# Optimization experiments

Measured on AMD Instinct MI355X. Metric: run time of the kernel, lower is better.

Reference implementation:

```python
import jax, jax.numpy as jnp
import numpy as np

GROUPS = 16
EPS = 1e-6


def conv1x1(x, w, b):
    # x: (B,C,N,K), w: (O,C), b: (O,)
    return jnp.einsum('oc,bcnk->bonk', w, x) + b[None, :, None, None]


def group_norm(x, gamma, beta):
    # GroupNorm(16, C, eps=1e-6, affine=True) over (C/g, N, K) per sample
    B, C, N, K = x.shape
    xg = x.reshape(B, GROUPS, C // GROUPS, N, K)
    mu = xg.mean(axis=(2, 3, 4), keepdims=True)
    var = xg.var(axis=(2, 3, 4), keepdims=True)
    xn = ((xg - mu) * jax.lax.rsqrt(var + EPS)).reshape(B, C, N, K)
    return xn * gamma[None, :, None, None] + beta[None, :, None, None]


def _gather_nbrs(x, idx):
    # x: (B,C,N), idx: (B,N,K) -> (B,C,N,K)
    return jax.vmap(lambda xb, ib: xb[:, ib])(x, idx)


def lse(coords_t, feats, idx, dist, w, b, g, bt):
    # LocalSpatialEncoding: coords_t (B,3,N), feats (B,C,N,1)
    nbr_coords = _gather_nbrs(coords_t, idx)                       # (B,3,N,K)
    ctr_coords = jnp.broadcast_to(coords_t[..., None], nbr_coords.shape)
    concat = jnp.concatenate(
        [ctr_coords, nbr_coords, ctr_coords - nbr_coords, dist[:, None]], axis=1)  # (B,10,N,K)
    enc = jax.nn.relu(group_norm(conv1x1(concat, w, b), g, bt))    # (B,C,N,K)
    nbr_feats = _gather_nbrs(feats[..., 0], idx)                   # (B,C,N,K)
    return jnp.concatenate([enc, nbr_feats], axis=1)               # (B,2C,N,K)


def attentive_pool(x, w, b, g, bt):
    # mean over K, then SharedMLP with GN+ReLU -> (B,O,N,1)
    m = x.mean(axis=-1, keepdims=True)
    return jax.nn.relu(group_norm(conv1x1(m, w, b), g, bt))


def setup_inputs() -> dict:
    B, N, K, D_IN, D_OUT = 2, 32768, 16, 72, 64
    H = D_OUT // 2  # 32
    key = jax.random.key(0)
    ks = jax.random.split(key, 24)

    def w(k, o, i):
        return jax.random.normal(k, (o, i), jnp.float32) * (1.0 / np.sqrt(i))

    inp = {
        'coords': jax.random.normal(ks[0], (B, N, 3), jnp.float32),
        'features': jax.random.normal(ks[1], (B, D_IN, N, 1), jnp.float32),
        'idx': jax.random.randint(ks[2], (B, N, K), 0, N, jnp.int32),
        'dist': jax.random.uniform(ks[3], (B, N, K), jnp.float32),
        # mlp1: d_in -> d_out//2, LeakyReLU(0.2)
        'w_mlp1': w(ks[4], H, D_IN), 'b_mlp1': jnp.zeros((H,), jnp.float32),
        # lse1 mlp: 10 -> H, GN+ReLU
        'w_lse1': w(ks[5], H, 10), 'b_lse1': jnp.zeros((H,), jnp.float32),
        'g_lse1': jnp.ones((H,), jnp.float32), 'bt_lse1': jnp.zeros((H,), jnp.float32),
        # pool1: d_out -> H, GN+ReLU
        'w_pool1': w(ks[6], H, D_OUT), 'b_pool1': jnp.zeros((H,), jnp.float32),
        'g_pool1': jnp.ones((H,), jnp.float32), 'bt_pool1': jnp.zeros((H,), jnp.float32),
        # lse2 mlp: 10 -> H
        'w_lse2': w(ks[7], H, 10), 'b_lse2': jnp.zeros((H,), jnp.float32),
        'g_lse2': jnp.ones((H,), jnp.float32), 'bt_lse2': jnp.zeros((H,), jnp.float32),
        # pool2: d_out -> d_out
        'w_pool2': w(ks[8], D_OUT, D_OUT), 'b_pool2': jnp.zeros((D_OUT,), jnp.float32),
        'g_pool2': jnp.ones((D_OUT,), jnp.float32), 'bt_pool2': jnp.zeros((D_OUT,), jnp.float32),
        # mlp2: d_out -> 2*d_out (no bn, no act)
        'w_mlp2': w(ks[9], 2 * D_OUT, D_OUT), 'b_mlp2': jnp.zeros((2 * D_OUT,), jnp.float32),
        # shortcut: d_in -> 2*d_out, GN, no act
        'w_sc': w(ks[10], 2 * D_OUT, D_IN), 'b_sc': jnp.zeros((2 * D_OUT,), jnp.float32),
        'g_sc': jnp.ones((2 * D_OUT,), jnp.float32), 'bt_sc': jnp.zeros((2 * D_OUT,), jnp.float32),
    }
    return inp


def reference(coords, features, idx, dist,
              w_mlp1, b_mlp1,
              w_lse1, b_lse1, g_lse1, bt_lse1,
              w_pool1, b_pool1, g_pool1, bt_pool1,
              w_lse2, b_lse2, g_lse2, bt_lse2,
              w_pool2, b_pool2, g_pool2, bt_pool2,
              w_mlp2, b_mlp2,
              w_sc, b_sc, g_sc, bt_sc):
    coords_t = coords.transpose(0, 2, 1)                        # (B,3,N)
    x = jax.nn.leaky_relu(conv1x1(features, w_mlp1, b_mlp1), 0.2)   # (B,32,N,1)
    x = lse(coords_t, x, idx, dist, w_lse1, b_lse1, g_lse1, bt_lse1)  # (B,64,N,K)
    x = attentive_pool(x, w_pool1, b_pool1, g_pool1, bt_pool1)        # (B,32,N,1)
    x = lse(coords_t, x, idx, dist, w_lse2, b_lse2, g_lse2, bt_lse2)  # (B,64,N,K)
    x = attentive_pool(x, w_pool2, b_pool2, g_pool2, bt_pool2)        # (B,64,N,1)
    main = conv1x1(x, w_mlp2, b_mlp2)                                 # (B,128,N,1)
    sc = group_norm(conv1x1(features, w_sc, b_sc), g_sc, bt_sc)       # (B,128,N,1)
    return jax.nn.leaky_relu(main + sc, 0.01)
```

## Files before the change

kernel.cpp:

```cpp
#include <hip/hip_runtime.h>
#include <hip/hip_fp16.h>

#define NN 32768
#define GEPS 1e-6f

__device__ __forceinline__ float wredsum(float v){
  v += __shfl_xor(v, 32); v += __shfl_xor(v, 16); v += __shfl_xor(v, 8);
  v += __shfl_xor(v, 4);  v += __shfl_xor(v, 2);  v += __shfl_xor(v, 1);
  return v;
}
__device__ __forceinline__ float eredsum(float v){
  v += __shfl_xor(v, 8); v += __shfl_xor(v, 16); v += __shfl_xor(v, 32);
  return v;
}
__device__ __forceinline__ float ecomb(float v){
  v += __shfl_xor(v, 1); v += __shfl_xor(v, 2); v += __shfl_xor(v, 4);
  return v;
}

__global__ void __launch_bounds__(256) f0_prep(
    const float* __restrict__ w_mlp1, const float* __restrict__ b_mlp1,
    const float* __restrict__ w_sc,   const float* __restrict__ b_sc,
    const float* __restrict__ w_pool1,const float* __restrict__ w_pool2,
    float* __restrict__ WallT, float* __restrict__ ball,
    float* __restrict__ wp1T,  float* __restrict__ wp2T)
{
  const int t0 = blockIdx.x*256 + threadIdx.x;
  const int stride = gridDim.x*256;
  for (int u=t0; u<72*160; u+=stride){
    int i = u/160, o = u - i*160;
    WallT[u] = (o < 128) ? w_sc[o*72+i] : w_mlp1[(o-128)*72+i];
  }
  for (int u=t0; u<160; u+=stride)
    ball[u] = (u < 128) ? b_sc[u] : b_mlp1[u-128];
  for (int u=t0; u<64*32; u+=stride){ int c=u>>5, o=u&31; wp1T[u] = w_pool1[o*64+c]; }
  for (int u=t0; u<64*64; u+=stride){ int c=u>>6, o=u&63; wp2T[u] = w_pool2[o*64+c]; }
}

__global__ void __launch_bounds__(256,2) k0_mlp1_scstats(
    const float* __restrict__ feat, const float* __restrict__ WallT,
    const float* __restrict__ ball,
    __half* __restrict__ X1, float* __restrict__ scS, float* __restrict__ scQ)
{
  __shared__ float xl[72][128];
  __shared__ float wl[72*32];
  __shared__ float ssl[128], sql[128];
  const int tid = threadIdx.x, lane = tid & 63;
  const int wid = __builtin_amdgcn_readfirstlane(tid >> 6);
  const int b   = __builtin_amdgcn_readfirstlane((int)blockIdx.x >> 8);
  const int n0  = ((int)blockIdx.x & 255) << 7;
  const int p0  = lane*2;

  for (int u=tid; u<72*128; u+=256){
    int c = u>>7, j = u&127;
    xl[c][j] = feat[(size_t)(b*72+c)*NN + n0 + j];
  }

#pragma unroll 1
  for (int pass=0; pass<5; ++pass){
    __syncthreads();
    for (int u=tid; u<2304; u+=256){
      int i = u>>5, c = u&31;
      wl[u] = WallT[i*160 + pass*32 + c];
    }
    __syncthreads();

    const int oc = pass*32 + wid*8;
    float a0[8], a1[8];
#pragma unroll
    for (int q=0;q<8;q++){ float bv = ball[oc+q]; a0[q]=bv; a1[q]=bv; }

    const float* wbase = wl + wid*8;
#pragma unroll
    for (int i=0;i<72;i++){
      const float2 x2 = *(const float2*)&xl[i][p0];
      const float4 w0 = *(const float4*)(wbase + i*32);
      const float4 w1 = *(const float4*)(wbase + i*32 + 4);
      a0[0]=fmaf(w0.x,x2.x,a0[0]); a1[0]=fmaf(w0.x,x2.y,a1[0]);
      a0[1]=fmaf(w0.y,x2.x,a0[1]); a1[1]=fmaf(w0.y,x2.y,a1[1]);
      a0[2]=fmaf(w0.z,x2.x,a0[2]); a1[2]=fmaf(w0.z,x2.y,a1[2]);
      a0[3]=fmaf(w0.w,x2.x,a0[3]); a1[3]=fmaf(w0.w,x2.y,a1[3]);
      a0[4]=fmaf(w1.x,x2.x,a0[4]); a1[4]=fmaf(w1.x,x2.y,a1[4]);
      a0[5]=fmaf(w1.y,x2.x,a0[5]); a1[5]=fmaf(w1.y,x2.y,a1[5]);
      a0[6]=fmaf(w1.z,x2.x,a0[6]); a1[6]=fmaf(w1.z,x2.y,a1[6]);
      a0[7]=fmaf(w1.w,x2.x,a0[7]); a1[7]=fmaf(w1.w,x2.y,a1[7]);
    }

    if (pass < 4){
#pragma unroll
      for (int q=0;q<8;q++){
        float s  = wredsum(a0[q]+a1[q]);
        float s2 = wredsum(a0[q]*a0[q] + a1[q]*a1[q]);
        if (lane==0){ ssl[oc+q] = s; sql[oc+q] = s2; }
      }
    } else {
      __syncthreads();
      float* xst = &xl[0][0];
#pragma unroll
      for (int q=0;q<8;q++){
        float v0 = a0[q], v1 = a1[q];
        v0 = v0 > 0.f ? v0 : 0.2f*v0;
        v1 = v1 > 0.f ? v1 : 0.2f*v1;
        float2 t; t.x=v0; t.y=v1;
        *(float2*)&xst[(wid*8+q)*130 + p0] = t;
      }
      __syncthreads();
      __half* xb = X1 + ((size_t)b*NN + n0)*32;
#pragma unroll
      for (int r=0;r<2;r++){
        int u = tid + r*256;
        int p = u>>2, co = (u&3)*8;
        __half2 h[4];
        h[0] = __floats2half2_rn(xst[(co+0)*130+p], xst[(co+1)*130+p]);
        h[1] = __floats2half2_rn(xst[(co+2)*130+p], xst[(co+3)*130+p]);
        h[2] = __floats2half2_rn(xst[(co+4)*130+p], xst[(co+5)*130+p]);
        h[3] = __floats2half2_rn(xst[(co+6)*130+p], xst[(co+7)*130+p]);
        *(uint4*)(xb + (size_t)p*32 + co) = *(uint4*)h;
      }
    }
  }

  if (tid < 128){
    atomicAdd(&scS[b*128+tid], ssl[tid]);
    atomicAdd(&scQ[b*128+tid], sql[tid]);
  }
}

__global__ void __launch_bounds__(256) k1_vmom(
    const float* __restrict__ coords, const int* __restrict__ idx,
    const float* __restrict__ dist, float* __restrict__ vm)
{
  __shared__ float red[4*65];
  const int tid = threadIdx.x, lane = tid & 63, wid = tid >> 6;
  const int gn = blockIdx.x*256 + tid;
  const int pt = gn >> 2, h = gn & 3;
  const int b = pt >> 15, n = pt & (NN-1);
  const size_t pb = (size_t)b*NN + n;
  const float c0 = coords[pb*3+0], c1 = coords[pb*3+1], c2 = coords[pb*3+2];

  int ja[4]; float da[4];
  {
    int4 j4 = *(const int4*)(idx + pb*16 + h*4);
    float4 d4 = *(const float4*)(dist + pb*16 + h*4);
    ja[0]=j4.x; ja[1]=j4.y; ja[2]=j4.z; ja[3]=j4.w;
    da[0]=d4.x; da[1]=d4.y; da[2]=d4.z; da[3]=d4.w;
  }

  float aS[10], aM[55];
#pragma unroll
  for (int i=0;i<10;i++) aS[i]=0.f;
#pragma unroll
  for (int i=0;i<55;i++) aM[i]=0.f;

#pragma unroll
  for (int k=0;k<4;k++){
    const float* nb = coords + ((size_t)b*NN + ja[k])*3;
    const float n0v=nb[0], n1v=nb[1], n2v=nb[2];
    const float v[10] = {c0,c1,c2,n0v,n1v,n2v,c0-n0v,c1-n1v,c2-n2v,da[k]};
#pragma unroll
    for (int i=0;i<10;i++){
      aS[i] += v[i];
#pragma unroll
      for (int j=i;j<10;j++)
        aM[i*10 - (i*(i-1))/2 + (j-i)] += v[i]*v[j];
    }
  }

#pragma unroll
  for (int i=0;i<10;i++){ float s = wredsum(aS[i]); if (lane==0) red[wid*65+i] = s; }
#pragma unroll
  for (int i=0;i<55;i++){ float s = wredsum(aM[i]); if (lane==0) red[wid*65+10+i] = s; }
  __syncthreads();
  if (tid < 65){
    float s = red[tid] + red[65+tid] + red[130+tid] + red[195+tid];
    const int bb = blockIdx.x >> 9;
    atomicAdd(&vm[bb*65+tid], s);
  }
}

__global__ void f1_fold(
    const float* __restrict__ w_lse1, const float* __restrict__ b_lse1,
    const float* __restrict__ g_lse1, const float* __restrict__ bt_lse1,
    const float* __restrict__ w_lse2, const float* __restrict__ b_lse2,
    const float* __restrict__ g_lse2, const float* __restrict__ bt_lse2,
    const float* __restrict__ vm,
    float* __restrict__ w1p, float* __restrict__ w2p)
{
  const int tid = threadIdx.x;
  const int half = tid >> 6;
  const int u = tid & 63, b = u >> 5, c = u & 31;
  const float* W  = half ? w_lse2  : w_lse1;
  const float* Bv = half ? b_lse2  : b_lse1;
  const float* G  = half ? g_lse2  : g_lse1;
  const float* Bt = half ? bt_lse2 : bt_lse1;
  float wr[10];
#pragma unroll
  for (int i=0;i<10;i++) wr[i] = W[c*10+i];
  const float* S = vm + b*65;
  const float* M = vm + b*65 + 10;
  float P = 0.f;
#pragma unroll
  for (int i=0;i<10;i++) P = fmaf(wr[i], S[i], P);
  float Q = 0.f;
#pragma unroll
  for (int i=0;i<10;i++){
#pragma unroll
    for (int j=i;j<10;j++){
      float m = M[i*10 - (i*(i-1))/2 + (j-i)];
      float t = wr[i]*wr[j]*m;
      Q += (i==j) ? t : 2.f*t;
    }
  }
  const float invNK = 1.f/((float)NN*16.f);
  const float bc = Bv[c];
  float mean = P*invNK + bc;
  float ey2  = (Q + 2.f*bc*P)*invNK + bc*bc;
  float mu = 0.5f*(mean + __shfl_xor(mean,1));
  float e2 = 0.5f*(ey2  + __shfl_xor(ey2, 1));
  float var = e2 - mu*mu;
  float rstd = rsqrtf(var + GEPS);
  float a = G[c]*rstd, d = Bt[c] - mu*a;
  float* out = (half ? w2p : w1p) + (b*32+c)*12;
#pragma unroll
  for (int i=0;i<10;i++) out[i] = wr[i]*a;
  out[10] = bc*a + d;
  out[11] = 0.f;
}

__global__ void __launch_bounds__(256,6) k2_lse1_pool1(
    const float* __restrict__ coords, const int* __restrict__ idx,
    const float* __restrict__ dist, const __half* __restrict__ X1,
    const float* __restrict__ w1p, const float* __restrict__ wp1T,
    const float* __restrict__ b_pool1,
    __half* __restrict__ Y1, float* __restrict__ p1S, float* __restrict__ p1Q)
{
  __shared__ float mfl[32*66];
  __shared__ float wlds[64*32];
  __shared__ float sl[32], ql[32];
  const int tid = threadIdx.x, lane = tid & 63;
  const int e = tid & 7;
  const int pl = tid >> 3;
  if (tid < 32){ sl[tid]=0.f; ql[tid]=0.f; }
  for (int u=tid; u<2048; u+=256) wlds[u] = wp1T[u];
  __syncthreads();
  const int b = __builtin_amdgcn_readfirstlane((int)blockIdx.x & 1);
  const int n = (((int)blockIdx.x >> 1) << 5) + pl;
  const size_t pb = (size_t)b*NN + n;
  float* mf = &mfl[pl*66];
  const float s16 = 0.0625f;

  {
    int ja[16];
    const int4* ip = (const int4*)(idx + pb*16);
#pragma unroll
    for (int k4=0;k4<4;k4++){
      int4 j4 = ip[k4];
      ja[k4*4+0]=j4.x; ja[k4*4+1]=j4.y; ja[k4*4+2]=j4.z; ja[k4*4+3]=j4.w;
    }
    float af0=0.f, af1=0.f, af2=0.f, af3=0.f;
    const __half* xb = X1 + (size_t)b*NN*32 + e*4;
#pragma unroll 4
    for (int k=0;k<16;k++){
      uint2 v = *(const uint2*)(xb + (size_t)ja[k]*32);
      __half2 h0 = *(__half2*)&v.x, h1 = *(__half2*)&v.y;
      float2 f0 = __half22float2(h0), f1 = __half22float2(h1);
      af0+=f0.x; af1+=f0.y; af2+=f1.x; af3+=f1.y;
    }
    mf[32+e*4+0]=af0*s16; mf[32+e*4+1]=af1*s16;
    mf[32+e*4+2]=af2*s16; mf[32+e*4+3]=af3*s16;
  }

  {
    int2 j2 = *(const int2*)(idx + pb*16 + e*2);
    float2 d2 = *(const float2*)(dist + pb*16 + e*2);
    const float* nb0 = coords + ((size_t)b*NN + j2.x)*3;
    const float* nb1 = coords + ((size_t)b*NN + j2.y)*3;
    const float nx0=nb0[0], ny0=nb0[1], nz0=nb0[2];
    const float nx1=nb1[0], ny1=nb1[1], nz1=nb1[2];
    const float c0=coords[pb*3], c1=coords[pb*3+1], c2=coords[pb*3+2];
    const float* wrow = w1p + (size_t)(b*32)*12;
#pragma unroll 1
    for (int cc=0;cc<4;cc++){
      float ptc[8];
#pragma unroll
      for (int q=0;q<8;q++){
        const float4* r4 = (const float4*)(wrow + (cc*8+q)*12);
        float4 ra=r4[0], rb=r4[1], rc=r4[2];
        const float t0=ra.x+rb.z, t1=ra.y+rb.w, t2=ra.z+rc.x;
        const float u0=ra.w-rb.z, u1=rb.x-rb.w, u2=rb.y-rc.x;
        const float wd=rc.y;
        float cb = rc.z;
        cb = fmaf(t0,c0,cb); cb = fmaf(t1,c1,cb); cb = fmaf(t2,c2,cb);
        float s0 = cb, s1 = cb;
        s0 = fmaf(u0,nx0,s0); s0 = fmaf(u1,ny0,s0); s0 = fmaf(u2,nz0,s0);
        s0 = fmaf(wd,d2.x,s0);
        s1 = fmaf(u0,nx1,s1); s1 = fmaf(u1,ny1,s1); s1 = fmaf(u2,nz1,s1);
        s1 = fmaf(wd,d2.y,s1);
        ptc[q] = fmaxf(s0,0.f) + fmaxf(s1,0.f);
      }
#pragma unroll
      for (int q=0;q<8;q++) ptc[q] = ecomb(ptc[q]);
      if ((e>>1)==cc){
        float v0 = (e&1) ? ptc[4] : ptc[0];
        float v1 = (e&1) ? ptc[5] : ptc[1];
        float v2 = (e&1) ? ptc[6] : ptc[2];
        float v3 = (e&1) ? ptc[7] : ptc[3];
        mf[e*4+0]=v0*s16; mf[e*4+1]=v1*s16;
        mf[e*4+2]=v2*s16; mf[e*4+3]=v3*s16;
      }
    }
  }
  __syncthreads();

  const int o0 = e*4;
  float yac[4];
  {
    const float4 b0 = *(const float4*)(b_pool1 + o0);
    yac[0]=b0.x; yac[1]=b0.y; yac[2]=b0.z; yac[3]=b0.w;
  }
#pragma unroll 4
  for (int c=0;c<64;c++){
    const float mc = mf[c];
    const float4 w0 = *(const float4*)(wlds + c*32 + o0);
    yac[0]=fmaf(w0.x,mc,yac[0]); yac[1]=fmaf(w0.y,mc,yac[1]);
    yac[2]=fmaf(w0.z,mc,yac[2]); yac[3]=fmaf(w0.w,mc,yac[3]);
  }
  {
    __half2 h[2];
    h[0] = __floats2half2_rn(yac[0], yac[1]);
    h[1] = __floats2half2_rn(yac[2], yac[3]);
    *(uint2*)(Y1 + pb*32 + o0) = *(uint2*)h;
  }
#pragma unroll
  for (int q=0;q<4;q++){
    float s  = eredsum(yac[q]);
    float s2 = eredsum(yac[q]*yac[q]);
    if (lane < 8){ atomicAdd(&sl[o0+q], s); atomicAdd(&ql[o0+q], s2); }
  }
  __syncthreads();
  if (tid<32){ atomicAdd(&p1S[b*32+tid], sl[tid]); atomicAdd(&p1Q[b*32+tid], ql[tid]); }
}

__global__ void __launch_bounds__(256,6) k4_lse2_pool2(
    const float* __restrict__ coords, const int* __restrict__ idx,
    const float* __restrict__ dist, const __half* __restrict__ Y1,
    const float* __restrict__ w2p, const float* __restrict__ wp2T,
    const float* __restrict__ b_pool2,
    const float* __restrict__ p1S, const float* __restrict__ p1Q,
    const float* __restrict__ g_p1, const float* __restrict__ bt_p1,
    float* __restrict__ Y2T, float* __restrict__ p2S, float* __restrict__ p2Q)
{
  __shared__ float mfl[32*66];
  __shared__ float wlds[64*64];
  __shared__ float sl[64], ql[64];
  __shared__ float al[32], dl[32];
  const int tid = threadIdx.x, lane = tid & 63;
  const int e = tid & 7;
  const int pl = tid >> 3;
  const int b = __builtin_amdgcn_readfirstlane((int)blockIdx.x & 1);
  if (tid < 64){ sl[tid]=0.f; ql[tid]=0.f; }
  if (tid >= 64 && tid < 96){
    const int c = tid - 64;
    float s = p1S[b*32+c], q = p1Q[b*32+c];
    s += __shfl_xor(s,1); q += __shfl_xor(q,1);
    const float inv = 1.f/(2.f*(float)NN);
    float mu = s*inv, e2 = q*inv, var = e2-mu*mu;
    float rstd = rsqrtf(var + GEPS);
    float a = g_p1[c]*rstd;
    al[c] = a; dl[c] = bt_p1[c] - mu*a;
  }
  for (int u=tid; u<4096; u+=256) wlds[u] = wp2T[u];
  __syncthreads();
  const int n0g = (((int)blockIdx.x >> 1) << 5);
  const int n = n0g + pl;
  const size_t pb = (size_t)b*NN + n;
  float* mf = &mfl[pl*66];
  const float s16 = 0.0625f;

  {
    const float a0g=al[e*4+0], a1g=al[e*4+1], a2g=al[e*4+2], a3g=al[e*4+3];
    const float d0g=dl[e*4+0], d1g=dl[e*4+1], d2g=dl[e*4+2], d3g=dl[e*4+3];
    int ja[16];
    const int4* ip = (const int4*)(idx + pb*16);
#pragma unroll
    for (int k4=0;k4<4;k4++){
      int4 j4 = ip[k4];
      ja[k4*4+0]=j4.x; ja[k4*4+1]=j4.y; ja[k4*4+2]=j4.z; ja[k4*4+3]=j4.w;
    }
    float af0=0.f, af1=0.f, af2=0.f, af3=0.f;
    const __half* yb = Y1 + (size_t)b*NN*32 + e*4;
#pragma unroll 4
    for (int k=0;k<16;k++){
      uint2 v = *(const uint2*)(yb + (size_t)ja[k]*32);
      __half2 h0 = *(__half2*)&v.x, h1 = *(__half2*)&v.y;
      float2 f0 = __half22float2(h0), f1 = __half22float2(h1);
      af0 += fmaxf(fmaf(f0.x, a0g, d0g), 0.f);
      af1 += fmaxf(fmaf(f0.y, a1g, d1g), 0.f);
      af2 += fmaxf(fmaf(f1.x, a2g, d2g), 0.f);
      af3 += fmaxf(fmaf(f1.y, a3g, d3g), 0.f);
    }
    mf[32+e*4+0]=af0*s16; mf[32+e*4+1]=af1*s16;
    mf[32+e*4+2]=af2*s16; mf[32+e*4+3]=af3*s16;
  }

  {
    int2 j2 = *(const int2*)(idx + pb*16 + e*2);
    float2 d2 = *(const float2*)(dist + pb*16 + e*2);
    const float* nb0 = coords + ((size_t)b*NN + j2.x)*3;
    const float* nb1 = coords + ((size_t)b*NN + j2.y)*3;
    const float nx0=nb0[0], ny0=nb0[1], nz0=nb0[2];
    const float nx1=nb1[0], ny1=nb1[1], nz1=nb1[2];
    const float c0=coords[pb*3], c1=coords[pb*3+1], c2=coords[pb*3+2];
    const float* wrow = w2p + (size_t)(b*32)*12;
#pragma unroll 1
    for (int cc=0;cc<4;cc++){
      float ptc[8];
#pragma unroll
      for (int q=0;q<8;q++){
        const float4* r4 = (const float4*)(wrow + (cc*8+q)*12);
        float4 ra=r4[0], rb=r4[1], rc=r4[2];
        const float t0=ra.x+rb.z, t1=ra.y+rb.w, t2=ra.z+rc.x;
        const float u0=ra.w-rb.z, u1=rb.x-rb.w, u2=rb.y-rc.x;
        const float wd=rc.y;
        float cb = rc.z;
        cb = fmaf(t0,c0,cb); cb = fmaf(t1,c1,cb); cb = fmaf(t2,c2,cb);
        float s0 = cb, s1 = cb;
        s0 = fmaf(u0,nx0,s0); s0 = fmaf(u1,ny0,s0); s0 = fmaf(u2,nz0,s0);
        s0 = fmaf(wd,d2.x,s0);
        s1 = fmaf(u0,nx1,s1); s1 = fmaf(u1,ny1,s1); s1 = fmaf(u2,nz1,s1);
        s1 = fmaf(wd,d2.y,s1);
        ptc[q] = fmaxf(s0,0.f) + fmaxf(s1,0.f);
      }
#pragma unroll
      for (int q=0;q<8;q++) ptc[q] = ecomb(ptc[q]);
      if ((e>>1)==cc){
        float v0 = (e&1) ? ptc[4] : ptc[0];
        float v1 = (e&1) ? ptc[5] : ptc[1];
        float v2 = (e&1) ? ptc[6] : ptc[2];
        float v3 = (e&1) ? ptc[7] : ptc[3];
        mf[e*4+0]=v0*s16; mf[e*4+1]=v1*s16;
        mf[e*4+2]=v2*s16; mf[e*4+3]=v3*s16;
      }
    }
  }
  __syncthreads();

  const int o0 = e*8;
  float yac[8];
  {
    const float4 b0 = *(const float4*)(b_pool2 + o0);
    const float4 b1 = *(const float4*)(b_pool2 + o0 + 4);
    yac[0]=b0.x; yac[1]=b0.y; yac[2]=b0.z; yac[3]=b0.w;
    yac[4]=b1.x; yac[5]=b1.y; yac[6]=b1.z; yac[7]=b1.w;
  }
#pragma unroll 4
  for (int c=0;c<64;c++){
    const float mc = mf[c];
    const float4 w0 = *(const float4*)(wlds + c*64 + o0);
    const float4 w1 = *(const float4*)(wlds + c*64 + o0 + 4);
    yac[0]=fmaf(w0.x,mc,yac[0]); yac[1]=fmaf(w0.y,mc,yac[1]);
    yac[2]=fmaf(w0.z,mc,yac[2]); yac[3]=fmaf(w0.w,mc,yac[3]);
    yac[4]=fmaf(w1.x,mc,yac[4]); yac[5]=fmaf(w1.y,mc,yac[5]);
    yac[6]=fmaf(w1.z,mc,yac[6]); yac[7]=fmaf(w1.w,mc,yac[7]);
  }
#pragma unroll
  for (int q=0;q<8;q++){
    float s  = eredsum(yac[q]);
    float s2 = eredsum(yac[q]*yac[q]);
    if (lane < 8){ atomicAdd(&sl[o0+q], s); atomicAdd(&ql[o0+q], s2); }
  }
  __syncthreads();
  float* ldsT = &mfl[0];
#pragma unroll
  for (int o=0;o<8;o++) ldsT[(o0+o)*33 + pl] = yac[o];
  __syncthreads();
#pragma unroll
  for (int r=0;r<8;r++){
    int u = tid + r*256;
    int ch = u >> 5, p = u & 31;
    Y2T[((size_t)(b*64+ch))*NN + n0g + p] = ldsT[ch*33 + p];
  }
  if (tid<64){ atomicAdd(&p2S[b*64+tid], sl[tid]); atomicAdd(&p2Q[b*64+tid], ql[tid]); }
}

__global__ void f3a_affines(
    const float* __restrict__ scS, const float* __restrict__ scQ,
    const float* __restrict__ g_sc, const float* __restrict__ bt_sc,
    const float* __restrict__ b_sc, const float* __restrict__ b_mlp2,
    const float* __restrict__ p2S, const float* __restrict__ p2Q,
    const float* __restrict__ g_p2, const float* __restrict__ bt_p2,
    float* __restrict__ ascT, float* __restrict__ cstF,
    float* __restrict__ a2F, float* __restrict__ d2F)
{
  const int tid = threadIdx.x;
  if (tid < 256){
    const int b = tid >> 7, c = tid & 127;
    float s = scS[b*128+c], q = scQ[b*128+c];
    s += __shfl_xor(s,1); q += __shfl_xor(q,1);
    s += __shfl_xor(s,2); q += __shfl_xor(q,2);
    s += __shfl_xor(s,4); q += __shfl_xor(q,4);
    const float inv = 1.f/(8.f*(float)NN);
    float mu = s*inv, e2 = q*inv, var = e2-mu*mu;
    float rstd = rsqrtf(var + GEPS);
    float a = g_sc[c]*rstd;
    ascT[tid] = a;
    cstF[tid] = b_mlp2[c] + a*b_sc[c] + (bt_sc[c] - mu*a);
  } else {
    const int t = tid - 256;
    const int b = t >> 6, c = t & 63;
    float s = p2S[b*64+c], q = p2Q[b*64+c];
    s += __shfl_xor(s,1); q += __shfl_xor(q,1);
    s += __shfl_xor(s,2); q += __shfl_xor(q,2);
    const float inv = 1.f/(4.f*(float)NN);
    float mu = s*inv, e2 = q*inv, var = e2-mu*mu;
    float rstd = rsqrtf(var + GEPS);
    float a = g_p2[c]*rstd;
    a2F[t] = a; d2F[t] = bt_p2[c] - mu*a;
  }
}

__global__ void __launch_bounds__(256) f3b_wcomb(
    const float* __restrict__ w_mlp2, const float* __restrict__ w_sc,
    const float* __restrict__ ascT, float* __restrict__ Wcomb)
{
  const int t0 = blockIdx.x*256 + threadIdx.x;
  const int stride = gridDim.x*256;
  for (int u=t0; u<2*136*128; u+=stride){
    int bb = u / 17408;
    int rr = u - bb*17408;
    int i = rr >> 7, o = rr & 127;
    Wcomb[u] = (i < 64) ? w_mlp2[o*64+i]
                        : w_sc[o*72 + (i-64)] * ascT[bb*128+o];
  }
}

__global__ void __launch_bounds__(256,4) k6_final(
    const float* __restrict__ feat, const float* __restrict__ Y2T,
    const float* __restrict__ Wcomb, const float* __restrict__ cstF,
    const float* __restrict__ a2F, const float* __restrict__ d2F,
    float* __restrict__ out)
{
  __shared__ float xl[34*64];
  __shared__ float wl[34*160];
  const int tid = threadIdx.x;
  const int tc = tid & 15;
  const int tp = tid >> 4;
  const int b  = __builtin_amdgcn_readfirstlane((int)blockIdx.x >> 9);
  const int n0 = ((int)blockIdx.x & 511) << 6;

  float acc[4][8];
#pragma unroll
  for (int q=0;q<8;q++){
    float bv = cstF[b*128 + tc*8 + q];
#pragma unroll
    for (int p=0;p<4;p++) acc[p][q] = bv;
  }

  const float* Wb = Wcomb + b*17408;
#pragma unroll 1
  for (int kk=0; kk<4; ++kk){
    __syncthreads();
    for (int u=tid; u<34*64; u+=256){
      int row = u>>6, j = u&63;
      int r = kk*34 + row;
      float v;
      if (r < 64){
        float y = Y2T[(size_t)(b*64+r)*NN + n0 + j];
        v = fmaxf(fmaf(y, a2F[b*64+r], d2F[b*64+r]), 0.f);
      } else {
        v = feat[(size_t)(b*72 + (r-64))*NN + n0 + j];
      }
      xl[u] = v;
    }
    for (int u=tid; u<34*128; u+=256){
      int row = u>>7, c = u&127;
      wl[row*160 + (c>>3)*10 + (c&7)] = Wb[(size_t)(kk*34+row)*128 + c];
    }
    __syncthreads();

#pragma unroll 2
    for (int i=0;i<34;i++){
      const float4 xa = *(const float4*)&xl[i*64 + tp*4];
      const float4 wa = *(const float4*)&wl[i*160 + tc*10];
      const float4 wb = *(const float4*)&wl[i*160 + tc*10 + 4];
      const float xs[4] = {xa.x,xa.y,xa.z,xa.w};
      const float wv[8] = {wa.x,wa.y,wa.z,wa.w,wb.x,wb.y,wb.z,wb.w};
#pragma unroll
      for (int p=0;p<4;p++)
#pragma unroll
        for (int q=0;q<8;q++)
          acc[p][q] = fmaf(wv[q], xs[p], acc[p][q]);
    }
  }

#pragma unroll
  for (int q=0;q<8;q++){
    const int ch = b*128 + tc*8 + q;
    float4 r0;
    float v;
    v = acc[0][q]; r0.x = v>0.f? v : 0.01f*v;
    v = acc[1][q]; r0.y = v>0.f? v : 0.01f*v;
    v = acc[2][q]; r0.z = v>0.f? v : 0.01f*v;
    v = acc[3][q]; r0.w = v>0.f? v : 0.01f*v;
    *(float4*)(out + (size_t)ch*NN + n0 + tp*4) = r0;
  }
}

extern "C" void kernel_launch(void* const* d_in, const int* in_sizes, int n_in,
                              void* d_out, int out_size, void* d_ws, size_t ws_size,
                              hipStream_t stream) {
  (void)in_sizes; (void)n_in; (void)out_size; (void)ws_size;
  const float* coords  = (const float*)d_in[0];
  const float* feats   = (const float*)d_in[1];
  const int*   idx     = (const int*)  d_in[2];
  const float* dist    = (const float*)d_in[3];
  const float* w_mlp1  = (const float*)d_in[4];
  const float* b_mlp1  = (const float*)d_in[5];
  const float* w_lse1  = (const float*)d_in[6];
  const float* b_lse1  = (const float*)d_in[7];
  const float* g_lse1  = (const float*)d_in[8];
  const float* bt_lse1 = (const float*)d_in[9];
  const float* w_pool1 = (const float*)d_in[10];
  const float* b_pool1 = (const float*)d_in[11];
  const float* g_pool1 = (const float*)d_in[12];
  const float* bt_pool1= (const float*)d_in[13];
  const float* w_lse2  = (const float*)d_in[14];
  const float* b_lse2  = (const float*)d_in[15];
  const float* g_lse2  = (const float*)d_in[16];
  const float* bt_lse2 = (const float*)d_in[17];
  const float* w_pool2 = (const float*)d_in[18];
  const float* b_pool2 = (const float*)d_in[19];
  const float* g_pool2 = (const float*)d_in[20];
  const float* bt_pool2= (const float*)d_in[21];
  const float* w_mlp2  = (const float*)d_in[22];
  const float* b_mlp2  = (const float*)d_in[23];
  const float* w_sc    = (const float*)d_in[24];
  const float* b_sc    = (const float*)d_in[25];
  const float* g_sc    = (const float*)d_in[26];
  const float* bt_sc   = (const float*)d_in[27];

  float* ws   = (float*)d_ws;
  float* scS  = ws;
  float* scQ  = ws + 256;
  float* vm   = ws + 512;
  float* p1S  = ws + 704;
  float* p1Q  = ws + 768;
  float* p2S  = ws + 832;
  float* p2Q  = ws + 960;
  float* w1p  = ws + 1280;
  float* w2p  = ws + 2048;
  float* wp1T = ws + 2816;
  float* wp2T = ws + 4864;
  float* ball = ws + 8960;
  float* cstF = ws + 9120;
  float* a2F  = ws + 9376;
  float* d2F  = ws + 9504;
  float* ascT = ws + 9632;
  float* WallT= ws + 9984;
  float* Wcomb= ws + 21504;
  __half* X1  = (__half*)(ws + 57344);
  __half* Y1  = (__half*)(ws + 57344 + (size_t)NN*32);
  float* Y2T  = ws + 57344 + (size_t)2*NN*32;

  hipMemsetAsync(d_ws, 0, 1088*sizeof(float), stream);

  f0_prep<<<32,256,0,stream>>>(w_mlp1,b_mlp1,w_sc,b_sc,w_pool1,w_pool2,
                               WallT,ball,wp1T,wp2T);
  k0_mlp1_scstats<<<512,256,0,stream>>>(feats, WallT, ball, X1, scS, scQ);
  k1_vmom<<<1024,256,0,stream>>>(coords, idx, dist, vm);
  f1_fold<<<1,128,0,stream>>>(w_lse1,b_lse1,g_lse1,bt_lse1,
                              w_lse2,b_lse2,g_lse2,bt_lse2,
                              vm, w1p, w2p);
  k2_lse1_pool1<<<2048,256,0,stream>>>(coords, idx, dist, X1, w1p, wp1T, b_pool1,
                                       Y1, p1S, p1Q);
  k4_lse2_pool2<<<2048,256,0,stream>>>(coords, idx, dist, Y1, w2p, wp2T, b_pool2,
                                       p1S, p1Q, g_pool1, bt_pool1,
                                       Y2T, p2S, p2Q);
  f3a_affines<<<1,384,0,stream>>>(scS,scQ,g_sc,bt_sc,b_sc,b_mlp2,
                                  p2S,p2Q,g_pool2,bt_pool2, ascT,cstF,a2F,d2F);
  f3b_wcomb<<<64,256,0,stream>>>(w_mlp2, w_sc, ascT, Wcomb);
  k6_final<<<1024,256,0,stream>>>(feats, Y2T, Wcomb, cstF, a2F, d2F, (float*)d_out);
}
```

Measured before the change: 236.1 us.

## Retile mlp1/shortcut-stats kernel to 64-point blocks with fp16 staging and direct stores

The first pointwise kernel now processes 64 points per block (1024 blocks) instead of 128. Input features are staged in shared memory as half2, which shrinks LDS use and allows higher occupancy (launch bounds 4). Each pass now computes 64 output channels, so there are 3 passes instead of 5, and the mlp1 output is written directly from registers as half vectors without a transposing shared-memory round trip. The cost is that input features are rounded to fp16 before the shortcut statistics and mlp1 are computed, which changes numerics. Half the warps also sit idle in the last pass.

```diff
diff --git a/kernel.cpp b/kernel.cpp
--- a/kernel.cpp
+++ b/kernel.cpp
@@ -15,6 +15,11 @@
 }
 __device__ __forceinline__ float ecomb(float v){
   v += __shfl_xor(v, 1); v += __shfl_xor(v, 2); v += __shfl_xor(v, 4);
+  return v;
+}
+__device__ __forceinline__ float hredsum(float v){
+  v += __shfl_xor(v, 16); v += __shfl_xor(v, 8);
+  v += __shfl_xor(v, 4);  v += __shfl_xor(v, 2);  v += __shfl_xor(v, 1);
   return v;
 }
 
@@ -37,45 +42,59 @@
   for (int u=t0; u<64*64; u+=stride){ int c=u>>6, o=u&63; wp2T[u] = w_pool2[o*64+c]; }
 }
 
-__global__ void __launch_bounds__(256,2) k0_mlp1_scstats(
+__global__ void __launch_bounds__(256,4) k0_mlp1_scstats(
     const float* __restrict__ feat, const float* __restrict__ WallT,
     const float* __restrict__ ball,
     __half* __restrict__ X1, float* __restrict__ scS, float* __restrict__ scQ)
 {
-  __shared__ float xl[72][128];
-  __shared__ float wl[72*32];
+  __shared__ __half2 xl2[72*32];
+  __shared__ float wl[72*64];
   __shared__ float ssl[128], sql[128];
-  const int tid = threadIdx.x, lane = tid & 63;
-  const int wid = __builtin_amdgcn_readfirstlane(tid >> 6);
-  const int b   = __builtin_amdgcn_readfirstlane((int)blockIdx.x >> 8);
-  const int n0  = ((int)blockIdx.x & 255) << 7;
-  const int p0  = lane*2;
-
-  for (int u=tid; u<72*128; u+=256){
-    int c = u>>7, j = u&127;
-    xl[c][j] = feat[(size_t)(b*72+c)*NN + n0 + j];
+  const int tid = threadIdx.x;
+  const int p2 = tid & 31;
+  const int g8 = tid >> 5;
+  const int b  = __builtin_amdgcn_readfirstlane((int)blockIdx.x >> 9);
+  const int n0 = ((int)blockIdx.x & 511) << 6;
+
+  for (int u=tid; u<72*32; u+=256){
+    int i = u>>5, pp = u&31;
+    float2 f = *(const float2*)(feat + (size_t)(b*72+i)*NN + n0 + pp*2);
+    xl2[u] = __floats2half2_rn(f.x, f.y);
   }
 
 #pragma unroll 1
-  for (int pass=0; pass<5; ++pass){
+  for (int pass=0; pass<3; ++pass){
+    const int cb  = pass*64;
     __syncthreads();
-    for (int u=tid; u<2304; u+=256){
-      int i = u>>5, c = u&31;
-      wl[u] = WallT[i*160 + pass*32 + c];
+    if (pass==2){
+      for (int u=tid; u<72*32; u+=256){
+        int i = u>>5, c = u&31;
+        wl[i*64 + c] = WallT[i*160 + 128 + c];
+      }
+    } else {
+      for (int u=tid; u<72*64; u+=256){
+        int i = u>>6, c = u&63;
+        wl[i*64 + c] = WallT[i*160 + cb + c];
+      }
     }
     __syncthreads();
 
-    const int oc = pass*32 + wid*8;
+    if (pass==2 && g8 >= 4){ continue; }
+
+    const int oc = g8*8;
     float a0[8], a1[8];
 #pragma unroll
-    for (int q=0;q<8;q++){ float bv = ball[oc+q]; a0[q]=bv; a1[q]=bv; }
-
-    const float* wbase = wl + wid*8;
+    for (int q=0;q<8;q++){
+      float bv = ball[cb + oc + q];
+      a0[q]=bv; a1[q]=bv;
+    }
+
+    const float* wbase = wl + oc;
 #pragma unroll
     for (int i=0;i<72;i++){
-      const float2 x2 = *(const float2*)&xl[i][p0];
-      const float4 w0 = *(const float4*)(wbase + i*32);
-      const float4 w1 = *(const float4*)(wbase + i*32 + 4);
+      const float2 x2 = __half22float2(xl2[i*32 + p2]);
+      const float4 w0 = *(const float4*)(wbase + i*64);
+      const float4 w1 = *(const float4*)(wbase + i*64 + 4);
       a0[0]=fmaf(w0.x,x2.x,a0[0]); a1[0]=fmaf(w0.x,x2.y,a1[0]);
       a0[1]=fmaf(w0.y,x2.x,a0[1]); a1[1]=fmaf(w0.y,x2.y,a1[1]);
       a0[2]=fmaf(w0.z,x2.x,a0[2]); a1[2]=fmaf(w0.z,x2.y,a1[2]);
@@ -86,40 +105,31 @@
       a0[7]=fmaf(w1.w,x2.x,a0[7]); a1[7]=fmaf(w1.w,x2.y,a1[7]);
     }
 
-    if (pass < 4){
+    if (pass < 2){
 #pragma unroll
       for (int q=0;q<8;q++){
-        float s  = wredsum(a0[q]+a1[q]);
-        float s2 = wredsum(a0[q]*a0[q] + a1[q]*a1[q]);
-        if (lane==0){ ssl[oc+q] = s; sql[oc+q] = s2; }
+        float s  = hredsum(a0[q]+a1[q]);
+        float s2 = hredsum(a0[q]*a0[q] + a1[q]*a1[q]);
+        if (p2==0){ ssl[cb+oc+q] = s; sql[cb+oc+q] = s2; }
       }
     } else {
-      __syncthreads();
-      float* xst = &xl[0][0];
-#pragma unroll
-      for (int q=0;q<8;q++){
-        float v0 = a0[q], v1 = a1[q];
-        v0 = v0 > 0.f ? v0 : 0.2f*v0;
-        v1 = v1 > 0.f ? v1 : 0.2f*v1;
-        float2 t; t.x=v0; t.y=v1;
-        *(float2*)&xst[(wid*8+q)*130 + p0] = t;
-      }
-      __syncthreads();
-      __half* xb = X1 + ((size_t)b*NN + n0)*32;
-#pragma unroll
-      for (int r=0;r<2;r++){
-        int u = tid + r*256;
-        int p = u>>2, co = (u&3)*8;
-        __half2 h[4];
-        h[0] = __floats2half2_rn(xst[(co+0)*130+p], xst[(co+1)*130+p]);
-        h[1] = __floats2half2_rn(xst[(co+2)*130+p], xst[(co+3)*130+p]);
-        h[2] = __floats2half2_rn(xst[(co+4)*130+p], xst[(co+5)*130+p]);
-        h[3] = __floats2half2_rn(xst[(co+6)*130+p], xst[(co+7)*130+p]);
-        *(uint4*)(xb + (size_t)p*32 + co) = *(uint4*)h;
-      }
-    }
-  }
-
+      __half2 h0[4], h1[4];
+#pragma unroll
+      for (int q=0;q<4;q++){
+        float v00 = a0[q*2],   v01 = a0[q*2+1];
+        float v10 = a1[q*2],   v11 = a1[q*2+1];
+        v00 = v00>0.f? v00 : 0.2f*v00;  v01 = v01>0.f? v01 : 0.2f*v01;
+        v10 = v10>0.f? v10 : 0.2f*v10;  v11 = v11>0.f? v11 : 0.2f*v11;
+        h0[q] = __floats2half2_rn(v00, v01);
+        h1[q] = __floats2half2_rn(v10, v11);
+      }
+      __half* xb = X1 + ((size_t)b*NN + n0 + p2*2)*32 + g8*8;
+      *(uint4*)(xb)      = *(uint4*)h0;
+      *(uint4*)(xb + 32) = *(uint4*)h1;
+    }
+  }
+
+  __syncthreads();
   if (tid < 128){
     atomicAdd(&scS[b*128+tid], ssl[tid]);
     atomicAdd(&scQ[b*128+tid], sql[tid]);
@@ -666,7 +676,7 @@
 
   f0_prep<<<32,256,0,stream>>>(w_mlp1,b_mlp1,w_sc,b_sc,w_pool1,w_pool2,
                                WallT,ball,wp1T,wp2T);
-  k0_mlp1_scstats<<<512,256,0,stream>>>(feats, WallT, ball, X1, scS, scQ);
+  k0_mlp1_scstats<<<1024,256,0,stream>>>(feats, WallT, ball, X1, scS, scQ);
   k1_vmom<<<1024,256,0,stream>>>(coords, idx, dist, vm);
   f1_fold<<<1,128,0,stream>>>(w_lse1,b_lse1,g_lse1,bt_lse1,
                               w_lse2,b_lse2,g_lse2,bt_lse2,
```

Result: no change. 235.4 us (-0.3%).
